# Kernel optimization log

Hardware: AMD Instinct MI355X
Metric: run time of the kernel (lower is better)

Reference implementation:

```python
import jax, jax.numpy as jnp
import numpy as np

N_NODES = 100000
N_EDGES = 600000
D_IN = 128
D_HID = 128
BLOCKS = 3


def setup_inputs() -> dict:
    key = jax.random.key(0)
    ks = jax.random.split(key, 8)
    x = jax.random.normal(ks[0], (N_NODES, D_IN), dtype=jnp.float32)
    edge_index = jax.random.randint(ks[1], (2, N_EDGES), 0, N_NODES, dtype=jnp.int64)
    s = 1.0 / np.sqrt(D_HID)
    # MLP params per GIN block: Linear1 [hid,in], Linear2 [hid,hid] (torch layout: [out,in])
    W1 = jax.random.uniform(ks[2], (BLOCKS, D_HID, D_IN), jnp.float32, -s, s)
    b1 = jax.random.uniform(ks[3], (BLOCKS, D_HID), jnp.float32, -s, s)
    W2 = jax.random.uniform(ks[4], (BLOCKS, D_HID, D_HID), jnp.float32, -s, s)
    b2 = jax.random.uniform(ks[5], (BLOCKS, D_HID), jnp.float32, -s, s)
    Wf = jax.random.uniform(ks[6], (1, D_HID), jnp.float32, -s, s)
    bf = jax.random.uniform(ks[7], (1,), jnp.float32, -s, s)
    return {"x": x, "edge_index": edge_index, "W1": W1, "b1": b1,
            "W2": W2, "b2": b2, "Wf": Wf, "bf": bf}


def reference(x, edge_index, W1, b1, W2, b2, Wf, bf):
    src, dst = edge_index[0], edge_index[1]
    n = x.shape[0]
    h = x
    for i in range(BLOCKS):
        # GIN aggregation: (1+eps)*x_i + sum over neighbors, eps=0
        agg = jax.ops.segment_sum(h[src], dst, num_segments=n)  # [N, d]
        z = h + agg
        # 2-layer MLP inside GINConv
        z = jax.nn.relu(z @ W1[i].T + b1[i])
        z = z @ W2[i].T + b2[i]
        # outer ReLU applied in Net.forward
        h = jax.nn.relu(z)
    return h @ Wf.T + bf  # [N, 1]
```

## Files before the change

kernel.cpp:

```cpp
#include <hip/hip_runtime.h>
#include <hip/hip_bf16.h>

typedef __bf16 bf16x8 __attribute__((ext_vector_type(8)));
typedef __bf16 bf16x2 __attribute__((ext_vector_type(2)));
typedef float f32x4 __attribute__((ext_vector_type(4)));

#define NN 100000
#define DD 128
#define NE 600000
#define SLOTS 32
#define DEGSTRIDE 16

__global__ void convert_bf16(const float4* __restrict__ in, __bf16* __restrict__ out, int n4) {
    int i = blockIdx.x * blockDim.x + threadIdx.x;
    if (i >= n4) return;
    float4 v = in[i];
    bf16x2 a, b;
    a[0] = (__bf16)v.x; a[1] = (__bf16)v.y;
    b[0] = (__bf16)v.z; b[1] = (__bf16)v.w;
    *reinterpret_cast<bf16x2*>(out + (size_t)i * 4)     = a;
    *reinterpret_cast<bf16x2*>(out + (size_t)i * 4 + 2) = b;
}

__global__ void clear_ints(int* __restrict__ p, int n) {
    int i = blockIdx.x * blockDim.x + threadIdx.x;
    if (i < n) p[i] = 0;
}

__global__ void fill_slots(const int* __restrict__ src, const int* __restrict__ dst,
                           int* __restrict__ degp, int* __restrict__ slots, int nE) {
    int e = blockIdx.x * blockDim.x + threadIdx.x;
    if (e >= nE) return;
    int d = dst[e];
    int pos = atomicAdd(&degp[(size_t)d * DEGSTRIDE], 1);
    if (pos < SLOTS) slots[(size_t)d * SLOTS + pos] = src[e];
}

__global__ __launch_bounds__(256) void aggregate(const __bf16* __restrict__ h,
                                                 const int* __restrict__ degp,
                                                 const int* __restrict__ slots,
                                                 __bf16* __restrict__ z, int N) {
    const int tid = threadIdx.x;
    const int grp = tid >> 4;
    const int lm  = tid & 15;
    const int n = blockIdx.x * 16 + grp;
    if (n >= N) return;
    const int off = lm * 8;

    const bf16x8 sv = *reinterpret_cast<const bf16x8*>(h + (size_t)n * DD + off);
    float acc[8];
#pragma unroll
    for (int i = 0; i < 8; ++i) acc[i] = (float)sv[i];

    int d = degp[(size_t)n * DEGSTRIDE]; if (d > SLOTS) d = SLOTS;
    const int* sl = slots + (size_t)n * SLOTS;
    const int d1 = d < 16 ? d : 16;
    int myidx = (lm < d1) ? sl[lm] : 0;

    int j = 0;
    if (j + 8 <= d1) {
        int s[8];
#pragma unroll
        for (int q = 0; q < 8; ++q) s[q] = __shfl(myidx, j + q, 16);
        bf16x8 v[8];
#pragma unroll
        for (int q = 0; q < 8; ++q) v[q] = *reinterpret_cast<const bf16x8*>(h + (size_t)s[q] * DD + off);
#pragma unroll
        for (int q = 0; q < 8; ++q)
#pragma unroll
            for (int i = 0; i < 8; ++i) acc[i] += (float)v[q][i];
        j += 8;
    }
    if (j + 4 <= d1) {
        int s[4];
#pragma unroll
        for (int q = 0; q < 4; ++q) s[q] = __shfl(myidx, j + q, 16);
        bf16x8 v[4];
#pragma unroll
        for (int q = 0; q < 4; ++q) v[q] = *reinterpret_cast<const bf16x8*>(h + (size_t)s[q] * DD + off);
#pragma unroll
        for (int q = 0; q < 4; ++q)
#pragma unroll
            for (int i = 0; i < 8; ++i) acc[i] += (float)v[q][i];
        j += 4;
    }
    for (; j < d1; ++j) {
        int s = __shfl(myidx, j, 16);
        bf16x8 v = *reinterpret_cast<const bf16x8*>(h + (size_t)s * DD + off);
#pragma unroll
        for (int i = 0; i < 8; ++i) acc[i] += (float)v[i];
    }

    if (d > 16) {
        const int d2 = d - 16;
        int myidx2 = (lm < d2) ? sl[16 + lm] : 0;
        j = 0;
        if (j + 8 <= d2) {
            int s[8];
#pragma unroll
            for (int q = 0; q < 8; ++q) s[q] = __shfl(myidx2, j + q, 16);
            bf16x8 v[8];
#pragma unroll
            for (int q = 0; q < 8; ++q) v[q] = *reinterpret_cast<const bf16x8*>(h + (size_t)s[q] * DD + off);
#pragma unroll
            for (int q = 0; q < 8; ++q)
#pragma unroll
                for (int i = 0; i < 8; ++i) acc[i] += (float)v[q][i];
            j += 8;
        }
        if (j + 4 <= d2) {
            int s[4];
#pragma unroll
            for (int q = 0; q < 4; ++q) s[q] = __shfl(myidx2, j + q, 16);
            bf16x8 v[4];
#pragma unroll
            for (int q = 0; q < 4; ++q) v[q] = *reinterpret_cast<const bf16x8*>(h + (size_t)s[q] * DD + off);
#pragma unroll
            for (int q = 0; q < 4; ++q)
#pragma unroll
                for (int i = 0; i < 8; ++i) acc[i] += (float)v[q][i];
            j += 4;
        }
        for (; j < d2; ++j) {
            int s = __shfl(myidx2, j, 16);
            bf16x8 v = *reinterpret_cast<const bf16x8*>(h + (size_t)s * DD + off);
#pragma unroll
            for (int i = 0; i < 8; ++i) acc[i] += (float)v[i];
        }
    }

    bf16x8 o;
#pragma unroll
    for (int i = 0; i < 8; ++i) o[i] = (__bf16)acc[i];
    *reinterpret_cast<bf16x8*>(z + (size_t)n * DD + off) = o;
}

template<bool LAST>
__global__ __launch_bounds__(512) void mlp_fused(const __bf16* __restrict__ A,
                                                 const float* __restrict__ W1,
                                                 const float* __restrict__ b1,
                                                 const float* __restrict__ W2,
                                                 const float* __restrict__ b2,
                                                 const float* __restrict__ Wf,
                                                 const float* __restrict__ bfp,
                                                 __bf16* __restrict__ Hout,
                                                 float* __restrict__ out, int N) {
    __shared__ __bf16 w1l[128 * 136];
    __shared__ __bf16 w2l[128 * 136];
    __shared__ __bf16 tl[128 * 136];
    const int tid = threadIdx.x;

    for (int i = tid; i < 128 * 128; i += 512) {
        int r = i >> 7, c = i & 127;
        w1l[r * 136 + c] = (__bf16)W1[i];
        w2l[r * 136 + c] = (__bf16)W2[i];
    }
    __syncthreads();

    const int wave = tid >> 6;
    const int lane = tid & 63;
    const int lm = lane & 15;
    const int kg = lane >> 4;
    const int rowL = wave * 16;
    const int row0 = blockIdx.x * 128 + rowL;

    f32x4 acc[8];
#pragma unroll
    for (int c = 0; c < 8; ++c) acc[c] = (f32x4){0.f, 0.f, 0.f, 0.f};

#pragma unroll
    for (int kk = 0; kk < 4; ++kk) {
        const int kbase = kk * 32 + kg * 8;
        int r = row0 + lm;
        if (r >= N) r = N - 1;
        const bf16x8 a = *reinterpret_cast<const bf16x8*>(A + (size_t)r * DD + kbase);
#pragma unroll
        for (int c = 0; c < 8; ++c) {
            const bf16x8 b = *reinterpret_cast<const bf16x8*>(&w1l[(c * 16 + lm) * 136 + kbase]);
            acc[c] = __builtin_amdgcn_mfma_f32_16x16x32_bf16(a, b, acc[c], 0, 0, 0);
        }
    }
#pragma unroll
    for (int c = 0; c < 8; ++c) {
        const int col = c * 16 + lm;
        const float bv = b1[col];
#pragma unroll
        for (int j = 0; j < 4; ++j) {
            float v = acc[c][j] + bv;
            tl[(rowL + kg * 4 + j) * 136 + col] = (__bf16)(v > 0.f ? v : 0.f);
        }
    }
    __syncthreads();

    f32x4 acc2[8];
#pragma unroll
    for (int c = 0; c < 8; ++c) acc2[c] = (f32x4){0.f, 0.f, 0.f, 0.f};

#pragma unroll
    for (int kk = 0; kk < 4; ++kk) {
        const int kbase = kk * 32 + kg * 8;
        const bf16x8 a2 = *reinterpret_cast<const bf16x8*>(&tl[(rowL + lm) * 136 + kbase]);
#pragma unroll
        for (int c = 0; c < 8; ++c) {
            const bf16x8 b = *reinterpret_cast<const bf16x8*>(&w2l[(c * 16 + lm) * 136 + kbase]);
            acc2[c] = __builtin_amdgcn_mfma_f32_16x16x32_bf16(a2, b, acc2[c], 0, 0, 0);
        }
    }

    if (!LAST) {
        __syncthreads();
#pragma unroll
        for (int c = 0; c < 8; ++c) {
            const int col = c * 16 + lm;
            const float bv = b2[col];
#pragma unroll
            for (int j = 0; j < 4; ++j) {
                float v = acc2[c][j] + bv;
                tl[(rowL + kg * 4 + j) * 136 + col] = (__bf16)(v > 0.f ? v : 0.f);
            }
        }
        __syncthreads();
        for (int i = tid; i < 128 * 16; i += 512) {
            int r = i >> 4, cc = (i & 15) * 8;
            int gr = blockIdx.x * 128 + r;
            if (gr < N) {
                bf16x8 v = *reinterpret_cast<const bf16x8*>(&tl[r * 136 + cc]);
                *reinterpret_cast<bf16x8*>(Hout + (size_t)gr * DD + cc) = v;
            }
        }
    } else {
        float wv[8];
#pragma unroll
        for (int c = 0; c < 8; ++c) wv[c] = Wf[c * 16 + lm];
        const float bias0 = bfp[0];
#pragma unroll
        for (int j = 0; j < 4; ++j) {
            float p = 0.f;
#pragma unroll
            for (int c = 0; c < 8; ++c) {
                const int col = c * 16 + lm;
                float v = acc2[c][j] + b2[col];
                p += (v > 0.f ? v : 0.f) * wv[c];
            }
            p += __shfl_xor(p, 1, 64);
            p += __shfl_xor(p, 2, 64);
            p += __shfl_xor(p, 4, 64);
            p += __shfl_xor(p, 8, 64);
            int row = row0 + kg * 4 + j;
            if (lm == 0 && row < N) out[row] = p + bias0;
        }
    }
}

extern "C" void kernel_launch(void* const* d_in, const int* in_sizes, int n_in,
                              void* d_out, int out_size, void* d_ws, size_t ws_size,
                              hipStream_t stream) {
    const float* x  = (const float*)d_in[0];
    const int*   ei = (const int*)d_in[1];
    const float* W1 = (const float*)d_in[2];
    const float* b1 = (const float*)d_in[3];
    const float* W2 = (const float*)d_in[4];
    const float* b2 = (const float*)d_in[5];
    const float* Wf = (const float*)d_in[6];
    const float* bf = (const float*)d_in[7];
    float* out = (float*)d_out;

    const int* src = ei;
    const int* dst = ei + NE;

    __bf16* Zb   = (__bf16*)d_ws;
    __bf16* Hb   = Zb + (size_t)NN * DD;
    __bf16* Xb   = Hb + (size_t)NN * DD;
    int*  slots  = (int*)(Xb + (size_t)NN * DD);
    int*  degp   = slots + (size_t)NN * SLOTS;

    const int aggGrid = (NN + 15) / 16;
    const int mlpGrid = (NN + 127) / 128;
    const int n4 = NN * DD / 4;

    convert_bf16<<<(n4 + 255) / 256, 256, 0, stream>>>((const float4*)x, Xb, n4);
    clear_ints<<<(NN * DEGSTRIDE + 255) / 256, 256, 0, stream>>>(degp, NN * DEGSTRIDE);
    fill_slots<<<(NE + 255) / 256, 256, 0, stream>>>(src, dst, degp, slots, NE);

    aggregate<<<aggGrid, 256, 0, stream>>>(Xb, degp, slots, Zb, NN);
    mlp_fused<false><<<mlpGrid, 512, 0, stream>>>(Zb, W1, b1, W2, b2, Wf, bf, Hb, out, NN);
    aggregate<<<aggGrid, 256, 0, stream>>>(Hb, degp, slots, Zb, NN);
    mlp_fused<false><<<mlpGrid, 512, 0, stream>>>(Zb, W1 + 128 * 128, b1 + 128, W2 + 128 * 128, b2 + 128,
                                                  Wf, bf, Hb, out, NN);
    aggregate<<<aggGrid, 256, 0, stream>>>(Hb, degp, slots, Zb, NN);
    mlp_fused<true><<<mlpGrid, 512, 0, stream>>>(Zb, W1 + 2 * 128 * 128, b1 + 2 * 128, W2 + 2 * 128 * 128,
                                                 b2 + 2 * 128, Wf, bf, Hb, out, NN);
}
```

Before: 227.7 us.

## Pre-convert weights to bf16, share one LDS weight buffer, simplify gather loop

```diff
diff --git a/kernel.cpp b/kernel.cpp
--- a/kernel.cpp
+++ b/kernel.cpp
@@ -11,20 +11,21 @@
 #define SLOTS 32
 #define DEGSTRIDE 16
 
-__global__ void convert_bf16(const float4* __restrict__ in, __bf16* __restrict__ out, int n4) {
+__global__ void prep(const float4* __restrict__ x4, __bf16* __restrict__ Xb,
+                     const float* __restrict__ W1, const float* __restrict__ W2,
+                     __bf16* __restrict__ W1b, __bf16* __restrict__ W2b,
+                     int* __restrict__ degp) {
     int i = blockIdx.x * blockDim.x + threadIdx.x;
-    if (i >= n4) return;
-    float4 v = in[i];
-    bf16x2 a, b;
-    a[0] = (__bf16)v.x; a[1] = (__bf16)v.y;
-    b[0] = (__bf16)v.z; b[1] = (__bf16)v.w;
-    *reinterpret_cast<bf16x2*>(out + (size_t)i * 4)     = a;
-    *reinterpret_cast<bf16x2*>(out + (size_t)i * 4 + 2) = b;
-}
-
-__global__ void clear_ints(int* __restrict__ p, int n) {
-    int i = blockIdx.x * blockDim.x + threadIdx.x;
-    if (i < n) p[i] = 0;
+    if (i < NN * DD / 4) {
+        float4 v = x4[i];
+        bf16x2 a, b;
+        a[0] = (__bf16)v.x; a[1] = (__bf16)v.y;
+        b[0] = (__bf16)v.z; b[1] = (__bf16)v.w;
+        *reinterpret_cast<bf16x2*>(Xb + (size_t)i * 4)     = a;
+        *reinterpret_cast<bf16x2*>(Xb + (size_t)i * 4 + 2) = b;
+    }
+    if (i < 3 * DD * DD) { W1b[i] = (__bf16)W1[i]; W2b[i] = (__bf16)W2[i]; }
+    if (i < NN * DEGSTRIDE) degp[i] = 0;
 }
 
 __global__ void fill_slots(const int* __restrict__ src, const int* __restrict__ dst,
@@ -57,75 +58,37 @@
     const int d1 = d < 16 ? d : 16;
     int myidx = (lm < d1) ? sl[lm] : 0;
 
-    int j = 0;
-    if (j + 8 <= d1) {
+    for (int base = 0; base < d1; base += 8) {
         int s[8];
 #pragma unroll
-        for (int q = 0; q < 8; ++q) s[q] = __shfl(myidx, j + q, 16);
+        for (int q = 0; q < 8; ++q) s[q] = __shfl(myidx, base + q, 16);
         bf16x8 v[8];
 #pragma unroll
         for (int q = 0; q < 8; ++q) v[q] = *reinterpret_cast<const bf16x8*>(h + (size_t)s[q] * DD + off);
 #pragma unroll
-        for (int q = 0; q < 8; ++q)
-#pragma unroll
-            for (int i = 0; i < 8; ++i) acc[i] += (float)v[q][i];
-        j += 8;
-    }
-    if (j + 4 <= d1) {
-        int s[4];
-#pragma unroll
-        for (int q = 0; q < 4; ++q) s[q] = __shfl(myidx, j + q, 16);
-        bf16x8 v[4];
-#pragma unroll
-        for (int q = 0; q < 4; ++q) v[q] = *reinterpret_cast<const bf16x8*>(h + (size_t)s[q] * DD + off);
-#pragma unroll
-        for (int q = 0; q < 4; ++q)
-#pragma unroll
-            for (int i = 0; i < 8; ++i) acc[i] += (float)v[q][i];
-        j += 4;
-    }
-    for (; j < d1; ++j) {
-        int s = __shfl(myidx, j, 16);
-        bf16x8 v = *reinterpret_cast<const bf16x8*>(h + (size_t)s * DD + off);
-#pragma unroll
-        for (int i = 0; i < 8; ++i) acc[i] += (float)v[i];
+        for (int q = 0; q < 8; ++q) {
+            const bool ok = (base + q) < d1;
+#pragma unroll
+            for (int i = 0; i < 8; ++i) acc[i] += ok ? (float)v[q][i] : 0.f;
+        }
     }
 
     if (d > 16) {
         const int d2 = d - 16;
         int myidx2 = (lm < d2) ? sl[16 + lm] : 0;
-        j = 0;
-        if (j + 8 <= d2) {
+        for (int base = 0; base < d2; base += 8) {
             int s[8];
 #pragma unroll
-            for (int q = 0; q < 8; ++q) s[q] = __shfl(myidx2, j + q, 16);
+            for (int q = 0; q < 8; ++q) s[q] = __shfl(myidx2, base + q, 16);
             bf16x8 v[8];
 #pragma unroll
             for (int q = 0; q < 8; ++q) v[q] = *reinterpret_cast<const bf16x8*>(h + (size_t)s[q] * DD + off);
 #pragma unroll
-            for (int q = 0; q < 8; ++q)
-#pragma unroll
-                for (int i = 0; i < 8; ++i) acc[i] += (float)v[q][i];
-            j += 8;
-        }
-        if (j + 4 <= d2) {
-            int s[4];
-#pragma unroll
-            for (int q = 0; q < 4; ++q) s[q] = __shfl(myidx2, j + q, 16);
-            bf16x8 v[4];
-#pragma unroll
-            for (int q = 0; q < 4; ++q) v[q] = *reinterpret_cast<const bf16x8*>(h + (size_t)s[q] * DD + off);
-#pragma unroll
-            for (int q = 0; q < 4; ++q)
-#pragma unroll
-                for (int i = 0; i < 8; ++i) acc[i] += (float)v[q][i];
-            j += 4;
-        }
-        for (; j < d2; ++j) {
-            int s = __shfl(myidx2, j, 16);
-            bf16x8 v = *reinterpret_cast<const bf16x8*>(h + (size_t)s * DD + off);
-#pragma unroll
-            for (int i = 0; i < 8; ++i) acc[i] += (float)v[i];
+            for (int q = 0; q < 8; ++q) {
+                const bool ok = (base + q) < d2;
+#pragma unroll
+                for (int i = 0; i < 8; ++i) acc[i] += ok ? (float)v[q][i] : 0.f;
+            }
         }
     }
 
@@ -136,24 +99,23 @@
 }
 
 template<bool LAST>
-__global__ __launch_bounds__(512) void mlp_fused(const __bf16* __restrict__ A,
-                                                 const float* __restrict__ W1,
-                                                 const float* __restrict__ b1,
-                                                 const float* __restrict__ W2,
-                                                 const float* __restrict__ b2,
-                                                 const float* __restrict__ Wf,
-                                                 const float* __restrict__ bfp,
-                                                 __bf16* __restrict__ Hout,
-                                                 float* __restrict__ out, int N) {
-    __shared__ __bf16 w1l[128 * 136];
-    __shared__ __bf16 w2l[128 * 136];
+__global__ __launch_bounds__(512, 4) void mlp_fused(const __bf16* __restrict__ A,
+                                                    const __bf16* __restrict__ W1b,
+                                                    const float* __restrict__ b1,
+                                                    const __bf16* __restrict__ W2b,
+                                                    const float* __restrict__ b2,
+                                                    const float* __restrict__ Wf,
+                                                    const float* __restrict__ bfp,
+                                                    __bf16* __restrict__ Hout,
+                                                    float* __restrict__ out, int N) {
+    __shared__ __bf16 wl[128 * 136];
     __shared__ __bf16 tl[128 * 136];
     const int tid = threadIdx.x;
 
-    for (int i = tid; i < 128 * 128; i += 512) {
-        int r = i >> 7, c = i & 127;
-        w1l[r * 136 + c] = (__bf16)W1[i];
-        w2l[r * 136 + c] = (__bf16)W2[i];
+    for (int i = tid; i < 2048; i += 512) {
+        int r = i >> 4, c = (i & 15) * 8;
+        *reinterpret_cast<bf16x8*>(&wl[r * 136 + c]) =
+            *reinterpret_cast<const bf16x8*>(W1b + (size_t)r * DD + c);
     }
     __syncthreads();
 
@@ -176,7 +138,7 @@
         const bf16x8 a = *reinterpret_cast<const bf16x8*>(A + (size_t)r * DD + kbase);
 #pragma unroll
         for (int c = 0; c < 8; ++c) {
-            const bf16x8 b = *reinterpret_cast<const bf16x8*>(&w1l[(c * 16 + lm) * 136 + kbase]);
+            const bf16x8 b = *reinterpret_cast<const bf16x8*>(&wl[(c * 16 + lm) * 136 + kbase]);
             acc[c] = __builtin_amdgcn_mfma_f32_16x16x32_bf16(a, b, acc[c], 0, 0, 0);
         }
     }
@@ -192,6 +154,13 @@
     }
     __syncthreads();
 
+    for (int i = tid; i < 2048; i += 512) {
+        int r = i >> 4, c = (i & 15) * 8;
+        *reinterpret_cast<bf16x8*>(&wl[r * 136 + c]) =
+            *reinterpret_cast<const bf16x8*>(W2b + (size_t)r * DD + c);
+    }
+    __syncthreads();
+
     f32x4 acc2[8];
 #pragma unroll
     for (int c = 0; c < 8; ++c) acc2[c] = (f32x4){0.f, 0.f, 0.f, 0.f};
@@ -202,13 +171,12 @@
         const bf16x8 a2 = *reinterpret_cast<const bf16x8*>(&tl[(rowL + lm) * 136 + kbase]);
 #pragma unroll
         for (int c = 0; c < 8; ++c) {
-            const bf16x8 b = *reinterpret_cast<const bf16x8*>(&w2l[(c * 16 + lm) * 136 + kbase]);
+            const bf16x8 b = *reinterpret_cast<const bf16x8*>(&wl[(c * 16 + lm) * 136 + kbase]);
             acc2[c] = __builtin_amdgcn_mfma_f32_16x16x32_bf16(a2, b, acc2[c], 0, 0, 0);
         }
     }
 
     if (!LAST) {
-        __syncthreads();
 #pragma unroll
         for (int c = 0; c < 8; ++c) {
             const int col = c * 16 + lm;
@@ -271,23 +239,24 @@
     __bf16* Zb   = (__bf16*)d_ws;
     __bf16* Hb   = Zb + (size_t)NN * DD;
     __bf16* Xb   = Hb + (size_t)NN * DD;
-    int*  slots  = (int*)(Xb + (size_t)NN * DD);
+    __bf16* W1b  = Xb + (size_t)NN * DD;
+    __bf16* W2b  = W1b + 3 * DD * DD;
+    int*  slots  = (int*)(W2b + 3 * DD * DD);
     int*  degp   = slots + (size_t)NN * SLOTS;
 
     const int aggGrid = (NN + 15) / 16;
     const int mlpGrid = (NN + 127) / 128;
-    const int n4 = NN * DD / 4;
-
-    convert_bf16<<<(n4 + 255) / 256, 256, 0, stream>>>((const float4*)x, Xb, n4);
-    clear_ints<<<(NN * DEGSTRIDE + 255) / 256, 256, 0, stream>>>(degp, NN * DEGSTRIDE);
+    const int prepGrid = (NN * DD / 4 + 255) / 256;
+
+    prep<<<prepGrid, 256, 0, stream>>>((const float4*)x, Xb, W1, W2, W1b, W2b, degp);
     fill_slots<<<(NE + 255) / 256, 256, 0, stream>>>(src, dst, degp, slots, NE);
 
     aggregate<<<aggGrid, 256, 0, stream>>>(Xb, degp, slots, Zb, NN);
-    mlp_fused<false><<<mlpGrid, 512, 0, stream>>>(Zb, W1, b1, W2, b2, Wf, bf, Hb, out, NN);
+    mlp_fused<false><<<mlpGrid, 512, 0, stream>>>(Zb, W1b, b1, W2b, b2, Wf, bf, Hb, out, NN);
     aggregate<<<aggGrid, 256, 0, stream>>>(Hb, degp, slots, Zb, NN);
-    mlp_fused<false><<<mlpGrid, 512, 0, stream>>>(Zb, W1 + 128 * 128, b1 + 128, W2 + 128 * 128, b2 + 128,
+    mlp_fused<false><<<mlpGrid, 512, 0, stream>>>(Zb, W1b + DD * DD, b1 + DD, W2b + DD * DD, b2 + DD,
                                                   Wf, bf, Hb, out, NN);
     aggregate<<<aggGrid, 256, 0, stream>>>(Hb, degp, slots, Zb, NN);
-    mlp_fused<true><<<mlpGrid, 512, 0, stream>>>(Zb, W1 + 2 * 128 * 128, b1 + 2 * 128, W2 + 2 * 128 * 128,
-                                                 b2 + 2 * 128, Wf, bf, Hb, out, NN);
-}
+    mlp_fused<true><<<mlpGrid, 512, 0, stream>>>(Zb, W1b + 2 * DD * DD, b1 + 2 * DD, W2b + 2 * DD * DD, b2 + 2 * DD,
+                                                 Wf, bf, Hb, out, NN);
+}
```

Result: faster. 196.8 us, median of 2 (-13.6%).
